# Performance work log

Hardware: AMD Instinct MI355X
Metric: run time of the kernel (lower is better)

## Reference

```python
import jax, jax.numpy as jnp
import numpy as np
from jax import lax

KS = [3, 5, 7, 9]
DS = [1, 2, 3, 4]
BN_EPS = 1e-5


def setup_inputs() -> dict:
    key = jax.random.key(0)
    ks = jax.random.split(key, 16)
    B, Cin, H, W = 16, 64, 256, 256
    Ce = 64  # out_channels // 2
    inp = {"x": jax.random.normal(ks[0], (B, Cin, H, W), jnp.float32)}
    for i, (k, _) in enumerate(zip(KS, DS)):
        fan_in = Cin * k * k
        inp[f"w{i}"] = jax.random.normal(ks[1 + i], (Ce, Cin, k, k), jnp.float32) / np.sqrt(fan_in)
        inp[f"b{i}"] = jnp.zeros((Ce,), jnp.float32)
    inp["bn_scale"] = jnp.ones((4, Ce), jnp.float32)
    inp["bn_bias"] = jnp.zeros((4, Ce), jnp.float32)
    inp["bn_mean"] = jax.random.normal(ks[5], (4, Ce), jnp.float32) * 0.1
    inp["bn_var"] = jax.random.uniform(ks[6], (4, Ce), jnp.float32, 0.5, 1.5)
    inp["gate_w"] = jax.random.normal(ks[7], (4, Cin), jnp.float32) / np.sqrt(Cin)
    inp["gate_b"] = jnp.zeros((4,), jnp.float32)
    return inp


def _expert(x, w, b, scale, bias, mean, var, k, d):
    pad = d * (k - 1) // 2
    y = lax.conv_general_dilated(
        x, w, window_strides=(2, 2), padding=[(pad, pad), (pad, pad)],
        rhs_dilation=(d, d), dimension_numbers=("NCHW", "OIHW", "NCHW"))
    y = y + b[None, :, None, None]
    inv = scale * lax.rsqrt(var + BN_EPS)
    y = y * inv[None, :, None, None] + (bias - mean * inv)[None, :, None, None]
    return jax.nn.gelu(y, approximate=False)


def reference(x, w0, b0, w1, b1, w2, b2, w3, b3,
              bn_scale, bn_bias, bn_mean, bn_var, gate_w, gate_b):
    B = x.shape[0]
    # Gate: global average pool -> linear -> softmax -> top-2 renormalized
    pooled = x.mean(axis=(2, 3))                    # (B, Cin)
    gates = jax.nn.softmax(pooled @ gate_w.T + gate_b, axis=1)  # (B, 4)
    top2_w, top2_idx = lax.top_k(gates, 2)
    top2_w = top2_w / (top2_w.sum(axis=1, keepdims=True) + 1e-8)
    # Dense compute of all 4 experts (faithful to original module)
    ws, bs = [w0, w1, w2, w3], [b0, b1, b2, b3]
    outs = [
        _expert(x, ws[i], bs[i], bn_scale[i], bn_bias[i], bn_mean[i], bn_var[i], KS[i], DS[i])
        for i in range(4)
    ]
    E = jnp.stack(outs, axis=1)                     # (B, 4, Ce, H/2, W/2)
    sel = jnp.take_along_axis(E, top2_idx[:, :, None, None, None], axis=1)  # (B,2,Ce,h,w)
    weighted = sel * top2_w[:, :, None, None, None]
    # concat top-2 along channel dim == reshape (B,2,Ce,h,w) -> (B,2*Ce,h,w)
    Bc, two, Ce, h, w = weighted.shape
    return weighted.reshape(Bc, two * Ce, h, w)
```

## Files before the change

### kernel.cpp

```cpp
#include <hip/hip_runtime.h>
#include <hip/hip_bf16.h>
#include <math.h>

#define CIN 64
#define CE  64
#define HH  256
#define WW  256
#define OHW 128
#define PW  288
#define PH  288

typedef __attribute__((ext_vector_type(8))) short bf16x8;
typedef __attribute__((ext_vector_type(4))) float f32x4;

static __device__ __forceinline__ unsigned short f2bf(float f) {
    __hip_bfloat16 h = __float2bfloat16(f);
    return *reinterpret_cast<unsigned short*>(&h);
}

#define GLOAD16(gsrc, ldst)                                                        \
    __builtin_amdgcn_global_load_lds(                                              \
        (const __attribute__((address_space(1))) void*)(gsrc),                     \
        (__attribute__((address_space(3))) void*)(ldst), 16, 0, 0)

template <bool PRE>
__global__ __launch_bounds__(256)
void poolcvt_kernel(const float* __restrict__ x, unsigned short* __restrict__ xbf,
                    float* __restrict__ partial) {
    int blk = blockIdx.x;
    int rc = blockIdx.y;
    int tid = threadIdx.x, lane = tid & 63, wv = tid >> 6;
    int c0 = lane * 4;
    const float* xb = x + (size_t)blk * 8 * (HH * WW);
    unsigned short* pl = xbf + (size_t)blk * (PW * PH) * 8;
    float s[8];
#pragma unroll
    for (int j = 0; j < 8; ++j) s[j] = 0.f;
#pragma unroll 1
    for (int rr = wv; rr < 32; rr += 4) {
        int h = rc * 32 + rr;
        float4 v[8];
#pragma unroll
        for (int j = 0; j < 8; ++j)
            v[j] = *reinterpret_cast<const float4*>(xb + (size_t)j * (HH * WW) + h * WW + c0);
#pragma unroll
        for (int j = 0; j < 8; ++j) s[j] += (v[j].x + v[j].y) + (v[j].z + v[j].w);
        if (PRE) {
            size_t o16 = ((size_t)(16 + h) * PW + 16 + c0);
            unsigned short u[4][8];
#pragma unroll
            for (int j = 0; j < 8; ++j) {
                u[0][j] = f2bf(v[j].x);
                u[1][j] = f2bf(v[j].y);
                u[2][j] = f2bf(v[j].z);
                u[3][j] = f2bf(v[j].w);
            }
#pragma unroll
            for (int cc = 0; cc < 4; ++cc)
                *reinterpret_cast<bf16x8*>(pl + (o16 + cc) * 8) =
                    *reinterpret_cast<const bf16x8*>(u[cc]);
        }
    }
    if (PRE) {
        bf16x8 z = (bf16x8)(short)0;
#pragma unroll 1
        for (int i = tid; i < 32 * 32; i += 256) {
            int rr = i >> 5, cc = i & 31;
            int pr = 16 + rc * 32 + rr;
            int pc = (cc < 16) ? cc : (256 + cc);
            *reinterpret_cast<bf16x8*>(pl + ((size_t)pr * PW + pc) * 8) = z;
        }
        if (rc == 0) {
#pragma unroll 1
            for (int i = tid; i < 16 * PW; i += 256)
                *reinterpret_cast<bf16x8*>(pl + (size_t)i * 8) = z;
        }
        if (rc == 7) {
#pragma unroll 1
            for (int i = tid; i < 16 * PW; i += 256)
                *reinterpret_cast<bf16x8*>(pl + ((size_t)(272 * PW) + i) * 8) = z;
        }
    }
#pragma unroll
    for (int j = 0; j < 8; ++j) {
#pragma unroll
        for (int m = 32; m >= 1; m >>= 1) s[j] += __shfl_xor(s[j], m, 64);
    }
    __shared__ float red[4][8];
    if (lane == 0) {
#pragma unroll
        for (int j = 0; j < 8; ++j) red[wv][j] = s[j];
    }
    __syncthreads();
    if (tid < 8) {
        int j = tid;
        float t = (red[0][j] + red[1][j]) + (red[2][j] + red[3][j]);
        partial[(blk * 8 + rc) * 8 + j] = t;
    }
}

__global__ __launch_bounds__(64)
void gate_kernel(const float* __restrict__ partial, const float* __restrict__ gw,
                 const float* __restrict__ gb, int* __restrict__ sel_idx,
                 float* __restrict__ sel_w) {
    int b = blockIdx.x;
    int c = threadIdx.x;
    float p = 0.f;
#pragma unroll
    for (int rc = 0; rc < 8; ++rc)
        p += partial[(((b * 8 + (c >> 3)) * 8) + rc) * 8 + (c & 7)];
    p *= (1.0f / (HH * WW));
    float l[4];
#pragma unroll
    for (int e = 0; e < 4; ++e) l[e] = p * gw[e * CIN + c];
#pragma unroll
    for (int m = 32; m >= 1; m >>= 1) {
#pragma unroll
        for (int e = 0; e < 4; ++e) l[e] += __shfl_xor(l[e], m, 64);
    }
    if (c == 0) {
        float g[4], s = 0.f;
#pragma unroll
        for (int e = 0; e < 4; ++e) l[e] += gb[e];
        float mx = fmaxf(fmaxf(l[0], l[1]), fmaxf(l[2], l[3]));
#pragma unroll
        for (int e = 0; e < 4; ++e) { g[e] = expf(l[e] - mx); s += g[e]; }
#pragma unroll
        for (int e = 0; e < 4; ++e) g[e] /= s;
        int i1 = 0;
        for (int e = 1; e < 4; ++e) if (g[e] > g[i1]) i1 = e;
        int i2 = -1;
        for (int e = 0; e < 4; ++e) {
            if (e == i1) continue;
            if (i2 < 0 || g[e] > g[i2]) i2 = e;
        }
        float den = g[i1] + g[i2] + 1e-8f;
        sel_idx[b * 2 + 0] = i1;
        sel_idx[b * 2 + 1] = i2;
        sel_w[b * 2 + 0] = g[i1] / den;
        sel_w[b * 2 + 1] = g[i2] / den;
    }
}

__global__ void order_kernel(const int* __restrict__ sel_idx, int* __restrict__ ord) {
    if (threadIdx.x == 0) {
        int pos = 0;
        const int pri[4] = {3, 2, 1, 0};
        for (int pi = 0; pi < 4; ++pi)
            for (int bs = 0; bs < 32; ++bs)
                if (sel_idx[bs] == pri[pi]) ord[pos++] = bs;
    }
}

__global__ __launch_bounds__(256)
void wprep_all_kernel(const float* __restrict__ w0, const float* __restrict__ w1,
                      const float* __restrict__ w2, const float* __restrict__ w3,
                      unsigned short* __restrict__ wq) {
    int cb = blockIdx.x;
    int y = blockIdx.y;
    const float* w;
    int g0, k, GE;
    size_t base;
    if (y < 3)       { w = w0; g0 = y;      k = 3; GE = 3;  base = 0; }
    else if (y < 10) { w = w1; g0 = y - 3;  k = 5; GE = 7;  base = 49152; }
    else if (y < 23) { w = w2; g0 = y - 10; k = 7; GE = 13; base = 163840; }
    else             { w = w3; g0 = y - 23; k = 9; GE = 21; base = 376832; }
    int k2 = k * k;
    int t = threadIdx.x, tl = t >> 6, co = t & 63;
    int tap = g0 * 4 + tl;
    unsigned short vals[8];
#pragma unroll
    for (int j = 0; j < 8; ++j) {
        float v = 0.f;
        if (tap < k2) v = w[(size_t)(co * CIN + cb * 8 + j) * k2 + tap];
        vals[j] = f2bf(v);
    }
    *reinterpret_cast<bf16x8*>(&wq[base + (size_t)(cb * GE + g0) * 2048 + t * 8]) =
        *reinterpret_cast<const bf16x8*>(vals);
}

template <int K, int D, int GE, bool EVEN, bool PRE>
__device__ __forceinline__ void conv_body(const float* __restrict__ xb,
                                          const unsigned short* __restrict__ xpb,
                                          const unsigned short* __restrict__ wq,
                                          unsigned short* __restrict__ xt,
                                          f32x4 acc[4][4],
                                          int ih0, int iw0, int lane, int wv, int tid) {
    constexpr int K2 = K * K;
    constexpr int TS = 31 + (K - 1) * D;
    constexpr int S = (TS + 1) / 2;
    constexpr int HPW = S * 8;
    constexpr int PITCH = 2 * HPW;
    constexpr int NRC = (TS + 1) / 2;
    constexpr int NEL = EVEN ? NRC * NRC : TS * 2 * S;
    constexpr int DH = EVEN ? D / 2 : 0;
    int p = lane & 15, hi = lane >> 4;

#pragma unroll 1
    for (int cb = 0; cb < 8; ++cb) {
        __syncthreads();
        if constexpr (PRE) {
            const unsigned short* xp = xpb + (size_t)cb * (PW * PH) * 8;
#pragma unroll 1
            for (int idx = tid; idx < NEL; idx += 256) {
                int ih, iw;
                if constexpr (EVEN) {
                    int r = idx / NRC, c = idx - r * NRC;
                    ih = ih0 + 16 + 2 * r;
                    iw = iw0 + 16 + 2 * c;
                } else {
                    int r = idx / (2 * S), rem = idx - r * (2 * S);
                    int half = rem >= S ? 1 : 0;
                    int sl = rem - half * S;
                    int c = 2 * sl + half;
                    c = min(c, TS - 1);
                    ih = ih0 + 16 + r;
                    iw = iw0 + 16 + c;
                }
                GLOAD16(xp + ((size_t)ih * PW + iw) * 8, &xt[idx * 8]);
            }
        } else {
            const float* xc8 = xb + (size_t)cb * 8 * (HH * WW);
#pragma unroll 1
            for (int idx = tid; idx < NEL; idx += 256) {
                int ih, iw;
                if constexpr (EVEN) {
                    int r = idx / NRC, c = idx - r * NRC;
                    ih = ih0 + 2 * r; iw = iw0 + 2 * c;
                } else {
                    int r = idx / (2 * S), rem = idx - r * (2 * S);
                    int half = rem >= S ? 1 : 0;
                    int sl = rem - half * S;
                    int c = min(2 * sl + half, TS - 1);
                    ih = ih0 + r; iw = iw0 + c;
                }
                int ihc = min(max(ih, 0), HH - 1), iwc = min(max(iw, 0), WW - 1);
                bool ok = ((unsigned)ih < (unsigned)HH) && ((unsigned)iw < (unsigned)WW);
                unsigned short u[8];
                const float* src = xc8 + ihc * WW + iwc;
#pragma unroll
                for (int j = 0; j < 8; ++j) u[j] = f2bf(ok ? src[(size_t)j * (HH * WW)] : 0.f);
                *reinterpret_cast<bf16x8*>(&xt[idx * 8]) = *reinterpret_cast<const bf16x8*>(u);
            }
        }
        __syncthreads();
        const unsigned short* wcb = wq + (size_t)cb * GE * 2048;
#pragma unroll 2
        for (int g = 0; g < GE; ++g) {
            int tap = g * 4 + hi;
            int tapc = tap < K2 ? tap : K2 - 1;
            int kh = tapc / K, kw = tapc % K;
            const unsigned short* wg = wcb + g * 2048 + hi * 512;
            bf16x8 a0 = *reinterpret_cast<const bf16x8*>(wg + p * 8);
            bf16x8 a1 = *reinterpret_cast<const bf16x8*>(wg + 128 + p * 8);
            bf16x8 a2 = *reinterpret_cast<const bf16x8*>(wg + 256 + p * 8);
            bf16x8 a3 = *reinterpret_cast<const bf16x8*>(wg + 384 + p * 8);
            if constexpr (EVEN) {
                int ec = p + DH * kw;
                int erb = wv * 4 + DH * kh;
#pragma unroll
                for (int j = 0; j < 4; ++j) {
                    const bf16x8 bf = *reinterpret_cast<const bf16x8*>(
                        &xt[((erb + j) * NRC + ec) * 8]);
                    acc[j][0] = __builtin_amdgcn_mfma_f32_16x16x32_bf16(a0, bf, acc[j][0], 0, 0, 0);
                    acc[j][1] = __builtin_amdgcn_mfma_f32_16x16x32_bf16(a1, bf, acc[j][1], 0, 0, 0);
                    acc[j][2] = __builtin_amdgcn_mfma_f32_16x16x32_bf16(a2, bf, acc[j][2], 0, 0, 0);
                    acc[j][3] = __builtin_amdgcn_mfma_f32_16x16x32_bf16(a3, bf, acc[j][3], 0, 0, 0);
                }
            } else {
                int ic = 2 * p + D * kw;
                int bbase = (ic & 1) * HPW + (ic >> 1) * 8;
                int irb = D * kh + wv * 8;
#pragma unroll
                for (int j = 0; j < 4; ++j) {
                    const bf16x8 bf = *reinterpret_cast<const bf16x8*>(
                        &xt[(irb + 2 * j) * PITCH + bbase]);
                    acc[j][0] = __builtin_amdgcn_mfma_f32_16x16x32_bf16(a0, bf, acc[j][0], 0, 0, 0);
                    acc[j][1] = __builtin_amdgcn_mfma_f32_16x16x32_bf16(a1, bf, acc[j][1], 0, 0, 0);
                    acc[j][2] = __builtin_amdgcn_mfma_f32_16x16x32_bf16(a2, bf, acc[j][2], 0, 0, 0);
                    acc[j][3] = __builtin_amdgcn_mfma_f32_16x16x32_bf16(a3, bf, acc[j][3], 0, 0, 0);
                }
            }
        }
    }
}

template <bool PRE>
__global__ __launch_bounds__(256, 4)
void conv_moe_kernel(const float* __restrict__ x, const unsigned short* __restrict__ xbf,
                     const unsigned short* __restrict__ wq,
                     const float* __restrict__ b0_, const float* __restrict__ b1_,
                     const float* __restrict__ b2_, const float* __restrict__ b3_,
                     const float* __restrict__ bns, const float* __restrict__ bnb,
                     const float* __restrict__ bnm, const float* __restrict__ bnv,
                     const int* __restrict__ sel_idx, const float* __restrict__ sel_w,
                     const int* __restrict__ ord, float* __restrict__ out) {
    __shared__ __align__(16) unsigned short xt[19600];

    int bidx = blockIdx.x;
    int bs = ord[bidx >> 6];
    int tile = bidx & 63;
    int b = bs >> 1, slot = bs & 1;
    int e = sel_idx[bs];
    float gwt = sel_w[bs];
    int oh0 = (tile >> 3) * 16, ow0 = (tile & 7) * 16;
    const float* xb = x + (size_t)b * CIN * HH * WW;
    const unsigned short* xpb = xbf + (size_t)b * 8 * (PW * PH) * 8;
    int tid = threadIdx.x, lane = tid & 63, wv = tid >> 6;
    int p = lane & 15, hi = lane >> 4;

    f32x4 acc[4][4];
#pragma unroll
    for (int j = 0; j < 4; ++j)
#pragma unroll
        for (int ct = 0; ct < 4; ++ct) acc[j][ct] = (f32x4){0.f, 0.f, 0.f, 0.f};

    switch (e) {
        case 0:
            conv_body<3, 1, 3, false, PRE>(xb, xpb, wq, xt, acc, oh0 * 2 - 1, ow0 * 2 - 1, lane, wv, tid);
            break;
        case 1:
            conv_body<5, 2, 7, true, PRE>(xb, xpb, wq + 49152, xt, acc, oh0 * 2 - 4, ow0 * 2 - 4, lane, wv, tid);
            break;
        case 2:
            conv_body<7, 3, 13, false, PRE>(xb, xpb, wq + 163840, xt, acc, oh0 * 2 - 9, ow0 * 2 - 9, lane, wv, tid);
            break;
        default:
            conv_body<9, 4, 21, true, PRE>(xb, xpb, wq + 376832, xt, acc, oh0 * 2 - 16, ow0 * 2 - 16, lane, wv, tid);
            break;
    }

    const float* be = (e == 0) ? b0_ : (e == 1) ? b1_ : (e == 2) ? b2_ : b3_;
    float* ob = out + (size_t)(b * 128 + slot * 64) * (OHW * OHW);
#pragma unroll
    for (int ct = 0; ct < 4; ++ct) {
#pragma unroll
        for (int reg = 0; reg < 4; ++reg) {
            int co = ct * 16 + hi * 4 + reg;
            float bias = be[co];
            float sc = bns[e * CE + co], bi = bnb[e * CE + co];
            float mn = bnm[e * CE + co], vr = bnv[e * CE + co];
            float inv = sc * rsqrtf(vr + 1e-5f);
            float beta = bi - mn * inv + bias * inv;
#pragma unroll
            for (int j = 0; j < 4; ++j) {
                float y = acc[j][ct][reg] * inv + beta;
                float gl = 0.5f * y * (1.0f + erff(y * 0.70710678118654752f));
                int oh = oh0 + wv * 4 + j, ow = ow0 + p;
                ob[(size_t)co * (OHW * OHW) + oh * OHW + ow] = gl * gwt;
            }
        }
    }
}

extern "C" void kernel_launch(void* const* d_in, const int* in_sizes, int n_in,
                              void* d_out, int out_size, void* d_ws, size_t ws_size,
                              hipStream_t stream) {
    const float* x   = (const float*)d_in[0];
    const float* w0  = (const float*)d_in[1];
    const float* b0  = (const float*)d_in[2];
    const float* w1  = (const float*)d_in[3];
    const float* b1  = (const float*)d_in[4];
    const float* w2  = (const float*)d_in[5];
    const float* b2  = (const float*)d_in[6];
    const float* w3  = (const float*)d_in[7];
    const float* b3  = (const float*)d_in[8];
    const float* bns = (const float*)d_in[9];
    const float* bnb = (const float*)d_in[10];
    const float* bnm = (const float*)d_in[11];
    const float* bnv = (const float*)d_in[12];
    const float* gw  = (const float*)d_in[13];
    const float* gb  = (const float*)d_in[14];
    float* out = (float*)d_out;

    char* ws = (char*)d_ws;
    float* partial = (float*)ws;
    int* sel_idx   = (int*)(ws + 32768);
    float* sel_w   = (float*)(ws + 32896);
    int* ord       = (int*)(ws + 33024);
    unsigned short* wq = (unsigned short*)(ws + 33280);
    unsigned short* xbf = (unsigned short*)(ws + 2097152);
    const size_t NEED = 2097152ull + (size_t)128 * PW * PH * 16;
    bool pre = ws_size >= NEED;

    if (pre) poolcvt_kernel<true><<<dim3(128, 8), 256, 0, stream>>>(x, xbf, partial);
    else     poolcvt_kernel<false><<<dim3(128, 8), 256, 0, stream>>>(x, xbf, partial);
    gate_kernel<<<dim3(16), 64, 0, stream>>>(partial, gw, gb, sel_idx, sel_w);
    order_kernel<<<dim3(1), 64, 0, stream>>>(sel_idx, ord);
    wprep_all_kernel<<<dim3(8, 44), 256, 0, stream>>>(w0, w1, w2, w3, wq);

    if (pre)
        conv_moe_kernel<true><<<dim3(2048), 256, 0, stream>>>(
            x, xbf, wq, b0, b1, b2, b3, bns, bnb, bnm, bnv, sel_idx, sel_w, ord, out);
    else
        conv_moe_kernel<false><<<dim3(2048), 256, 0, stream>>>(
            x, xbf, wq, b0, b1, b2, b3, bns, bnb, bnm, bnv, sel_idx, sel_w, ord, out);
}
```

Measured before the change: 305.2 us.

## Register-prefetch next channel block's input tile during MFMA compute

Replaces direct global-to-LDS loads with register staging. The next channel block's tile is loaded into registers while MFMAs run on the current LDS tile, and its global offsets are precomputed once outside the loop. This is meant to hide global load latency behind compute. In exchange it raises register pressure (ITER bf16x8 values per thread), so launch bounds drop from 4 to 3 blocks per SM, which lowers occupancy.

```diff
diff --git a/kernel.cpp b/kernel.cpp
--- a/kernel.cpp
+++ b/kernel.cpp
@@ -17,11 +17,6 @@
     __hip_bfloat16 h = __float2bfloat16(f);
     return *reinterpret_cast<unsigned short*>(&h);
 }
-
-#define GLOAD16(gsrc, ldst)                                                        \
-    __builtin_amdgcn_global_load_lds(                                              \
-        (const __attribute__((address_space(1))) void*)(gsrc),                     \
-        (__attribute__((address_space(3))) void*)(ldst), 16, 0, 0)
 
 template <bool PRE>
 __global__ __launch_bounds__(256)
@@ -193,33 +188,96 @@
     constexpr int PITCH = 2 * HPW;
     constexpr int NRC = (TS + 1) / 2;
     constexpr int NEL = EVEN ? NRC * NRC : TS * 2 * S;
+    constexpr int ITER = (NEL + 255) / 256;
     constexpr int DH = EVEN ? D / 2 : 0;
+    constexpr size_t PLANE = (size_t)PW * PH * 8;
     int p = lane & 15, hi = lane >> 4;
 
-#pragma unroll 1
-    for (int cb = 0; cb < 8; ++cb) {
-        __syncthreads();
-        if constexpr (PRE) {
-            const unsigned short* xp = xpb + (size_t)cb * (PW * PH) * 8;
-#pragma unroll 1
-            for (int idx = tid; idx < NEL; idx += 256) {
-                int ih, iw;
+    if constexpr (PRE) {
+        int gofs[ITER];
+#pragma unroll
+        for (int i = 0; i < ITER; ++i) {
+            int idx = tid + i * 256;
+            if (idx > NEL - 1) idx = NEL - 1;
+            int ih, iw;
+            if constexpr (EVEN) {
+                int r = idx / NRC, c = idx - r * NRC;
+                ih = ih0 + 16 + 2 * r;
+                iw = iw0 + 16 + 2 * c;
+            } else {
+                int r = idx / (2 * S), rem = idx - r * (2 * S);
+                int half = rem >= S ? 1 : 0;
+                int sl = rem - half * S;
+                int c = 2 * sl + half;
+                if (c > TS - 1) c = TS - 1;
+                ih = ih0 + 16 + r;
+                iw = iw0 + 16 + c;
+            }
+            gofs[i] = (ih * PW + iw) * 8;
+        }
+        bf16x8 st[ITER];
+#pragma unroll
+        for (int i = 0; i < ITER; ++i)
+            st[i] = *reinterpret_cast<const bf16x8*>(xpb + gofs[i]);
+
+#pragma unroll 1
+        for (int cb = 0; cb < 8; ++cb) {
+            __syncthreads();
+#pragma unroll
+            for (int i = 0; i < ITER; ++i) {
+                int idx = tid + i * 256;
+                if (idx < NEL) *reinterpret_cast<bf16x8*>(&xt[idx * 8]) = st[i];
+            }
+            __syncthreads();
+            if (cb < 7) {
+                const unsigned short* pn = xpb + (size_t)(cb + 1) * PLANE;
+#pragma unroll
+                for (int i = 0; i < ITER; ++i)
+                    st[i] = *reinterpret_cast<const bf16x8*>(pn + gofs[i]);
+            }
+            const unsigned short* wcb = wq + (size_t)cb * GE * 2048;
+#pragma unroll 2
+            for (int g = 0; g < GE; ++g) {
+                int tap = g * 4 + hi;
+                int tapc = tap < K2 ? tap : K2 - 1;
+                int kh = tapc / K, kw = tapc % K;
+                const unsigned short* wg = wcb + g * 2048 + hi * 512;
+                bf16x8 a0 = *reinterpret_cast<const bf16x8*>(wg + p * 8);
+                bf16x8 a1 = *reinterpret_cast<const bf16x8*>(wg + 128 + p * 8);
+                bf16x8 a2 = *reinterpret_cast<const bf16x8*>(wg + 256 + p * 8);
+                bf16x8 a3 = *reinterpret_cast<const bf16x8*>(wg + 384 + p * 8);
                 if constexpr (EVEN) {
-                    int r = idx / NRC, c = idx - r * NRC;
-                    ih = ih0 + 16 + 2 * r;
-                    iw = iw0 + 16 + 2 * c;
+                    int ec = p + DH * kw;
+                    int erb = wv * 4 + DH * kh;
+#pragma unroll
+                    for (int j = 0; j < 4; ++j) {
+                        const bf16x8 bf = *reinterpret_cast<const bf16x8*>(
+                            &xt[((erb + j) * NRC + ec) * 8]);
+                        acc[j][0] = __builtin_amdgcn_mfma_f32_16x16x32_bf16(a0, bf, acc[j][0], 0, 0, 0);
+                        acc[j][1] = __builtin_amdgcn_mfma_f32_16x16x32_bf16(a1, bf, acc[j][1], 0, 0, 0);
+                        acc[j][2] = __builtin_amdgcn_mfma_f32_16x16x32_bf16(a2, bf, acc[j][2], 0, 0, 0);
+                        acc[j][3] = __builtin_amdgcn_mfma_f32_16x16x32_bf16(a3, bf, acc[j][3], 0, 0, 0);
+                    }
                 } else {
-                    int r = idx / (2 * S), rem = idx - r * (2 * S);
-                    int half = rem >= S ? 1 : 0;
-                    int sl = rem - half * S;
-                    int c = 2 * sl + half;
-                    c = min(c, TS - 1);
-                    ih = ih0 + 16 + r;
-                    iw = iw0 + 16 + c;
+                    int ic = 2 * p + D * kw;
+                    int bbase = (ic & 1) * HPW + (ic >> 1) * 8;
+                    int irb = D * kh + wv * 8;
+#pragma unroll
+                    for (int j = 0; j < 4; ++j) {
+                        const bf16x8 bf = *reinterpret_cast<const bf16x8*>(
+                            &xt[(irb + 2 * j) * PITCH + bbase]);
+                        acc[j][0] = __builtin_amdgcn_mfma_f32_16x16x32_bf16(a0, bf, acc[j][0], 0, 0, 0);
+                        acc[j][1] = __builtin_amdgcn_mfma_f32_16x16x32_bf16(a1, bf, acc[j][1], 0, 0, 0);
+                        acc[j][2] = __builtin_amdgcn_mfma_f32_16x16x32_bf16(a2, bf, acc[j][2], 0, 0, 0);
+                        acc[j][3] = __builtin_amdgcn_mfma_f32_16x16x32_bf16(a3, bf, acc[j][3], 0, 0, 0);
+                    }
                 }
-                GLOAD16(xp + ((size_t)ih * PW + iw) * 8, &xt[idx * 8]);
-            }
-        } else {
+            }
+        }
+    } else {
+#pragma unroll 1
+        for (int cb = 0; cb < 8; ++cb) {
+            __syncthreads();
             const float* xc8 = xb + (size_t)cb * 8 * (HH * WW);
 #pragma unroll 1
             for (int idx = tid; idx < NEL; idx += 256) {
@@ -242,51 +300,51 @@
                 for (int j = 0; j < 8; ++j) u[j] = f2bf(ok ? src[(size_t)j * (HH * WW)] : 0.f);
                 *reinterpret_cast<bf16x8*>(&xt[idx * 8]) = *reinterpret_cast<const bf16x8*>(u);
             }
-        }
-        __syncthreads();
-        const unsigned short* wcb = wq + (size_t)cb * GE * 2048;
+            __syncthreads();
+            const unsigned short* wcb = wq + (size_t)cb * GE * 2048;
 #pragma unroll 2
-        for (int g = 0; g < GE; ++g) {
-            int tap = g * 4 + hi;
-            int tapc = tap < K2 ? tap : K2 - 1;
-            int kh = tapc / K, kw = tapc % K;
-            const unsigned short* wg = wcb + g * 2048 + hi * 512;
-            bf16x8 a0 = *reinterpret_cast<const bf16x8*>(wg + p * 8);
-            bf16x8 a1 = *reinterpret_cast<const bf16x8*>(wg + 128 + p * 8);
-            bf16x8 a2 = *reinterpret_cast<const bf16x8*>(wg + 256 + p * 8);
-            bf16x8 a3 = *reinterpret_cast<const bf16x8*>(wg + 384 + p * 8);
-            if constexpr (EVEN) {
-                int ec = p + DH * kw;
-                int erb = wv * 4 + DH * kh;
-#pragma unroll
-                for (int j = 0; j < 4; ++j) {
-                    const bf16x8 bf = *reinterpret_cast<const bf16x8*>(
-                        &xt[((erb + j) * NRC + ec) * 8]);
-                    acc[j][0] = __builtin_amdgcn_mfma_f32_16x16x32_bf16(a0, bf, acc[j][0], 0, 0, 0);
-                    acc[j][1] = __builtin_amdgcn_mfma_f32_16x16x32_bf16(a1, bf, acc[j][1], 0, 0, 0);
-                    acc[j][2] = __builtin_amdgcn_mfma_f32_16x16x32_bf16(a2, bf, acc[j][2], 0, 0, 0);
-                    acc[j][3] = __builtin_amdgcn_mfma_f32_16x16x32_bf16(a3, bf, acc[j][3], 0, 0, 0);
+            for (int g = 0; g < GE; ++g) {
+                int tap = g * 4 + hi;
+                int tapc = tap < K2 ? tap : K2 - 1;
+                int kh = tapc / K, kw = tapc % K;
+                const unsigned short* wg = wcb + g * 2048 + hi * 512;
+                bf16x8 a0 = *reinterpret_cast<const bf16x8*>(wg + p * 8);
+                bf16x8 a1 = *reinterpret_cast<const bf16x8*>(wg + 128 + p * 8);
+                bf16x8 a2 = *reinterpret_cast<const bf16x8*>(wg + 256 + p * 8);
+                bf16x8 a3 = *reinterpret_cast<const bf16x8*>(wg + 384 + p * 8);
+                if constexpr (EVEN) {
+                    int ec = p + DH * kw;
+                    int erb = wv * 4 + DH * kh;
+#pragma unroll
+                    for (int j = 0; j < 4; ++j) {
+                        const bf16x8 bf = *reinterpret_cast<const bf16x8*>(
+                            &xt[((erb + j) * NRC + ec) * 8]);
+                        acc[j][0] = __builtin_amdgcn_mfma_f32_16x16x32_bf16(a0, bf, acc[j][0], 0, 0, 0);
+                        acc[j][1] = __builtin_amdgcn_mfma_f32_16x16x32_bf16(a1, bf, acc[j][1], 0, 0, 0);
+                        acc[j][2] = __builtin_amdgcn_mfma_f32_16x16x32_bf16(a2, bf, acc[j][2], 0, 0, 0);
+                        acc[j][3] = __builtin_amdgcn_mfma_f32_16x16x32_bf16(a3, bf, acc[j][3], 0, 0, 0);
+                    }
+                } else {
+                    int ic = 2 * p + D * kw;
+                    int bbase = (ic & 1) * HPW + (ic >> 1) * 8;
+                    int irb = D * kh + wv * 8;
+#pragma unroll
+                    for (int j = 0; j < 4; ++j) {
+                        const bf16x8 bf = *reinterpret_cast<const bf16x8*>(
+                            &xt[(irb + 2 * j) * PITCH + bbase]);
+                        acc[j][0] = __builtin_amdgcn_mfma_f32_16x16x32_bf16(a0, bf, acc[j][0], 0, 0, 0);
+                        acc[j][1] = __builtin_amdgcn_mfma_f32_16x16x32_bf16(a1, bf, acc[j][1], 0, 0, 0);
+                        acc[j][2] = __builtin_amdgcn_mfma_f32_16x16x32_bf16(a2, bf, acc[j][2], 0, 0, 0);
+                        acc[j][3] = __builtin_amdgcn_mfma_f32_16x16x32_bf16(a3, bf, acc[j][3], 0, 0, 0);
+                    }
                 }
-            } else {
-                int ic = 2 * p + D * kw;
-                int bbase = (ic & 1) * HPW + (ic >> 1) * 8;
-                int irb = D * kh + wv * 8;
-#pragma unroll
-                for (int j = 0; j < 4; ++j) {
-                    const bf16x8 bf = *reinterpret_cast<const bf16x8*>(
-                        &xt[(irb + 2 * j) * PITCH + bbase]);
-                    acc[j][0] = __builtin_amdgcn_mfma_f32_16x16x32_bf16(a0, bf, acc[j][0], 0, 0, 0);
-                    acc[j][1] = __builtin_amdgcn_mfma_f32_16x16x32_bf16(a1, bf, acc[j][1], 0, 0, 0);
-                    acc[j][2] = __builtin_amdgcn_mfma_f32_16x16x32_bf16(a2, bf, acc[j][2], 0, 0, 0);
-                    acc[j][3] = __builtin_amdgcn_mfma_f32_16x16x32_bf16(a3, bf, acc[j][3], 0, 0, 0);
-                }
             }
         }
     }
 }
 
 template <bool PRE>
-__global__ __launch_bounds__(256, 4)
+__global__ __launch_bounds__(256, 3)
 void conv_moe_kernel(const float* __restrict__ x, const unsigned short* __restrict__ xbf,
                      const unsigned short* __restrict__ wq,
                      const float* __restrict__ b0_, const float* __restrict__ b1_,
```

After: 307.1 us. Within noise of the previous version (+0.6%).

## Stage conv weights through double-buffered LDS with async loads in PRE path

Applied to the files above, without the earlier changes.

In the prepadded-bf16 path, each weight group is now copied into a double-buffered LDS region with global_load_lds, one group ahead of the MFMA loop. MFMA A-operands are read from LDS instead of directly from global memory. A manual vmcnt wait plus barrier per group replaces the two syncthreads per channel block, and tap indices are stepped incrementally instead of recomputed with divisions. The input tile load is now only waited on at the first group barrier, so it can overlap with that barrier point. The cost is a full barrier per weight group, 8 KB more LDS per block, and launch bounds dropped from 4 to 3 blocks per CU, which lowers occupancy.

```diff
diff --git a/kernel.cpp b/kernel.cpp
--- a/kernel.cpp
+++ b/kernel.cpp
@@ -9,6 +9,7 @@
 #define OHW 128
 #define PW  288
 #define PH  288
+#define WOFF 19600
 
 typedef __attribute__((ext_vector_type(8))) short bf16x8;
 typedef __attribute__((ext_vector_type(4))) float f32x4;
@@ -183,7 +184,7 @@
 __device__ __forceinline__ void conv_body(const float* __restrict__ xb,
                                           const unsigned short* __restrict__ xpb,
                                           const unsigned short* __restrict__ wq,
-                                          unsigned short* __restrict__ xt,
+                                          unsigned short* __restrict__ lds,
                                           f32x4 acc[4][4],
                                           int ih0, int iw0, int lane, int wv, int tid) {
     constexpr int K2 = K * K;
@@ -194,12 +195,19 @@
     constexpr int NRC = (TS + 1) / 2;
     constexpr int NEL = EVEN ? NRC * NRC : TS * 2 * S;
     constexpr int DH = EVEN ? D / 2 : 0;
+    constexpr int NPH = 8 * GE;
     int p = lane & 15, hi = lane >> 4;
 
-#pragma unroll 1
-    for (int cb = 0; cb < 8; ++cb) {
-        __syncthreads();
-        if constexpr (PRE) {
+    if constexpr (PRE) {
+        GLOAD16(wq + tid * 8, &lds[WOFF + tid * 8]);
+        const unsigned short* wrun = wq + 2048;
+        int ph = 1;
+        int par = 0;
+
+#pragma unroll 1
+        for (int cb = 0; cb < 8; ++cb) {
+            asm volatile("s_waitcnt vmcnt(0)" ::: "memory");
+            __builtin_amdgcn_s_barrier();
             const unsigned short* xp = xpb + (size_t)cb * (PW * PH) * 8;
 #pragma unroll 1
             for (int idx = tid; idx < NEL; idx += 256) {
@@ -213,13 +221,64 @@
                     int half = rem >= S ? 1 : 0;
                     int sl = rem - half * S;
                     int c = 2 * sl + half;
-                    c = min(c, TS - 1);
+                    if (c > TS - 1) c = TS - 1;
                     ih = ih0 + 16 + r;
                     iw = iw0 + 16 + c;
                 }
-                GLOAD16(xp + ((size_t)ih * PW + iw) * 8, &xt[idx * 8]);
-            }
-        } else {
+                GLOAD16(xp + ((size_t)ih * PW + iw) * 8, &lds[idx * 8]);
+            }
+            int kh = hi / K, kw = hi % K;
+#pragma unroll 2
+            for (int g = 0; g < GE; ++g) {
+                asm volatile("s_waitcnt vmcnt(0)" ::: "memory");
+                __builtin_amdgcn_s_barrier();
+                if (ph < NPH) {
+                    GLOAD16(wrun + tid * 8, &lds[WOFF + (par ^ 1) * 2048 + tid * 8]);
+                    wrun += 2048;
+                    ++ph;
+                }
+                const unsigned short* wl = &lds[WOFF + par * 2048 + hi * 512 + p * 8];
+                bf16x8 a0 = *reinterpret_cast<const bf16x8*>(wl);
+                bf16x8 a1 = *reinterpret_cast<const bf16x8*>(wl + 128);
+                bf16x8 a2 = *reinterpret_cast<const bf16x8*>(wl + 256);
+                bf16x8 a3 = *reinterpret_cast<const bf16x8*>(wl + 384);
+                int khc = min(kh, K - 1);
+                if constexpr (EVEN) {
+                    int ec = p + DH * kw;
+                    int erb = wv * 4 + DH * khc;
+#pragma unroll
+                    for (int j = 0; j < 4; ++j) {
+                        const bf16x8 bf = *reinterpret_cast<const bf16x8*>(
+                            &lds[((erb + j) * NRC + ec) * 8]);
+                        acc[j][0] = __builtin_amdgcn_mfma_f32_16x16x32_bf16(a0, bf, acc[j][0], 0, 0, 0);
+                        acc[j][1] = __builtin_amdgcn_mfma_f32_16x16x32_bf16(a1, bf, acc[j][1], 0, 0, 0);
+                        acc[j][2] = __builtin_amdgcn_mfma_f32_16x16x32_bf16(a2, bf, acc[j][2], 0, 0, 0);
+                        acc[j][3] = __builtin_amdgcn_mfma_f32_16x16x32_bf16(a3, bf, acc[j][3], 0, 0, 0);
+                    }
+                } else {
+                    int ic = 2 * p + D * kw;
+                    int bbase = (ic & 1) * HPW + (ic >> 1) * 8;
+                    int irb = D * khc + wv * 8;
+#pragma unroll
+                    for (int j = 0; j < 4; ++j) {
+                        const bf16x8 bf = *reinterpret_cast<const bf16x8*>(
+                            &lds[(irb + 2 * j) * PITCH + bbase]);
+                        acc[j][0] = __builtin_amdgcn_mfma_f32_16x16x32_bf16(a0, bf, acc[j][0], 0, 0, 0);
+                        acc[j][1] = __builtin_amdgcn_mfma_f32_16x16x32_bf16(a1, bf, acc[j][1], 0, 0, 0);
+                        acc[j][2] = __builtin_amdgcn_mfma_f32_16x16x32_bf16(a2, bf, acc[j][2], 0, 0, 0);
+                        acc[j][3] = __builtin_amdgcn_mfma_f32_16x16x32_bf16(a3, bf, acc[j][3], 0, 0, 0);
+                    }
+                }
+                kw += 4;
+                if (kw >= K) { kw -= K; ++kh; }
+                if (K == 3 && kw >= K) { kw -= K; ++kh; }
+                par ^= 1;
+            }
+        }
+    } else {
+#pragma unroll 1
+        for (int cb = 0; cb < 8; ++cb) {
+            __syncthreads();
             const float* xc8 = xb + (size_t)cb * 8 * (HH * WW);
 #pragma unroll 1
             for (int idx = tid; idx < NEL; idx += 256) {
@@ -240,53 +299,53 @@
                 const float* src = xc8 + ihc * WW + iwc;
 #pragma unroll
                 for (int j = 0; j < 8; ++j) u[j] = f2bf(ok ? src[(size_t)j * (HH * WW)] : 0.f);
-                *reinterpret_cast<bf16x8*>(&xt[idx * 8]) = *reinterpret_cast<const bf16x8*>(u);
-            }
-        }
-        __syncthreads();
-        const unsigned short* wcb = wq + (size_t)cb * GE * 2048;
+                *reinterpret_cast<bf16x8*>(&lds[idx * 8]) = *reinterpret_cast<const bf16x8*>(u);
+            }
+            __syncthreads();
+            const unsigned short* wcb = wq + (size_t)cb * GE * 2048;
 #pragma unroll 2
-        for (int g = 0; g < GE; ++g) {
-            int tap = g * 4 + hi;
-            int tapc = tap < K2 ? tap : K2 - 1;
-            int kh = tapc / K, kw = tapc % K;
-            const unsigned short* wg = wcb + g * 2048 + hi * 512;
-            bf16x8 a0 = *reinterpret_cast<const bf16x8*>(wg + p * 8);
-            bf16x8 a1 = *reinterpret_cast<const bf16x8*>(wg + 128 + p * 8);
-            bf16x8 a2 = *reinterpret_cast<const bf16x8*>(wg + 256 + p * 8);
-            bf16x8 a3 = *reinterpret_cast<const bf16x8*>(wg + 384 + p * 8);
-            if constexpr (EVEN) {
-                int ec = p + DH * kw;
-                int erb = wv * 4 + DH * kh;
-#pragma unroll
-                for (int j = 0; j < 4; ++j) {
-                    const bf16x8 bf = *reinterpret_cast<const bf16x8*>(
-                        &xt[((erb + j) * NRC + ec) * 8]);
-                    acc[j][0] = __builtin_amdgcn_mfma_f32_16x16x32_bf16(a0, bf, acc[j][0], 0, 0, 0);
-                    acc[j][1] = __builtin_amdgcn_mfma_f32_16x16x32_bf16(a1, bf, acc[j][1], 0, 0, 0);
-                    acc[j][2] = __builtin_amdgcn_mfma_f32_16x16x32_bf16(a2, bf, acc[j][2], 0, 0, 0);
-                    acc[j][3] = __builtin_amdgcn_mfma_f32_16x16x32_bf16(a3, bf, acc[j][3], 0, 0, 0);
+            for (int g = 0; g < GE; ++g) {
+                int tap = g * 4 + hi;
+                int tapc = tap < K2 ? tap : K2 - 1;
+                int kh = tapc / K, kw = tapc % K;
+                const unsigned short* wg = wcb + g * 2048 + hi * 512;
+                bf16x8 a0 = *reinterpret_cast<const bf16x8*>(wg + p * 8);
+                bf16x8 a1 = *reinterpret_cast<const bf16x8*>(wg + 128 + p * 8);
+                bf16x8 a2 = *reinterpret_cast<const bf16x8*>(wg + 256 + p * 8);
+                bf16x8 a3 = *reinterpret_cast<const bf16x8*>(wg + 384 + p * 8);
+                if constexpr (EVEN) {
+                    int ec = p + (D / 2) * kw;
+                    int erb = wv * 4 + (D / 2) * kh;
+#pragma unroll
+                    for (int j = 0; j < 4; ++j) {
+                        const bf16x8 bf = *reinterpret_cast<const bf16x8*>(
+                            &lds[((erb + j) * NRC + ec) * 8]);
+                        acc[j][0] = __builtin_amdgcn_mfma_f32_16x16x32_bf16(a0, bf, acc[j][0], 0, 0, 0);
+                        acc[j][1] = __builtin_amdgcn_mfma_f32_16x16x32_bf16(a1, bf, acc[j][1], 0, 0, 0);
+                        acc[j][2] = __builtin_amdgcn_mfma_f32_16x16x32_bf16(a2, bf, acc[j][2], 0, 0, 0);
+                        acc[j][3] = __builtin_amdgcn_mfma_f32_16x16x32_bf16(a3, bf, acc[j][3], 0, 0, 0);
+                    }
+                } else {
+                    int ic = 2 * p + D * kw;
+                    int bbase = (ic & 1) * HPW + (ic >> 1) * 8;
+                    int irb = D * kh + wv * 8;
+#pragma unroll
+                    for (int j = 0; j < 4; ++j) {
+                        const bf16x8 bf = *reinterpret_cast<const bf16x8*>(
+                            &lds[(irb + 2 * j) * PITCH + bbase]);
+                        acc[j][0] = __builtin_amdgcn_mfma_f32_16x16x32_bf16(a0, bf, acc[j][0], 0, 0, 0);
+                        acc[j][1] = __builtin_amdgcn_mfma_f32_16x16x32_bf16(a1, bf, acc[j][1], 0, 0, 0);
+                        acc[j][2] = __builtin_amdgcn_mfma_f32_16x16x32_bf16(a2, bf, acc[j][2], 0, 0, 0);
+                        acc[j][3] = __builtin_amdgcn_mfma_f32_16x16x32_bf16(a3, bf, acc[j][3], 0, 0, 0);
+                    }
                 }
-            } else {
-                int ic = 2 * p + D * kw;
-                int bbase = (ic & 1) * HPW + (ic >> 1) * 8;
-                int irb = D * kh + wv * 8;
-#pragma unroll
-                for (int j = 0; j < 4; ++j) {
-                    const bf16x8 bf = *reinterpret_cast<const bf16x8*>(
-                        &xt[(irb + 2 * j) * PITCH + bbase]);
-                    acc[j][0] = __builtin_amdgcn_mfma_f32_16x16x32_bf16(a0, bf, acc[j][0], 0, 0, 0);
-                    acc[j][1] = __builtin_amdgcn_mfma_f32_16x16x32_bf16(a1, bf, acc[j][1], 0, 0, 0);
-                    acc[j][2] = __builtin_amdgcn_mfma_f32_16x16x32_bf16(a2, bf, acc[j][2], 0, 0, 0);
-                    acc[j][3] = __builtin_amdgcn_mfma_f32_16x16x32_bf16(a3, bf, acc[j][3], 0, 0, 0);
-                }
             }
         }
     }
 }
 
 template <bool PRE>
-__global__ __launch_bounds__(256, 4)
+__global__ __launch_bounds__(256, 3)
 void conv_moe_kernel(const float* __restrict__ x, const unsigned short* __restrict__ xbf,
                      const unsigned short* __restrict__ wq,
                      const float* __restrict__ b0_, const float* __restrict__ b1_,
@@ -295,7 +354,7 @@
                      const float* __restrict__ bnm, const float* __restrict__ bnv,
                      const int* __restrict__ sel_idx, const float* __restrict__ sel_w,
                      const int* __restrict__ ord, float* __restrict__ out) {
-    __shared__ __align__(16) unsigned short xt[19600];
+    __shared__ __align__(16) unsigned short lds[WOFF + 4096];
 
     int bidx = blockIdx.x;
     int bs = ord[bidx >> 6];
@@ -317,16 +376,16 @@
 
     switch (e) {
         case 0:
-            conv_body<3, 1, 3, false, PRE>(xb, xpb, wq, xt, acc, oh0 * 2 - 1, ow0 * 2 - 1, lane, wv, tid);
+            conv_body<3, 1, 3, false, PRE>(xb, xpb, wq, lds, acc, oh0 * 2 - 1, ow0 * 2 - 1, lane, wv, tid);
             break;
         case 1:
-            conv_body<5, 2, 7, true, PRE>(xb, xpb, wq + 49152, xt, acc, oh0 * 2 - 4, ow0 * 2 - 4, lane, wv, tid);
+            conv_body<5, 2, 7, true, PRE>(xb, xpb, wq + 49152, lds, acc, oh0 * 2 - 4, ow0 * 2 - 4, lane, wv, tid);
             break;
         case 2:
-            conv_body<7, 3, 13, false, PRE>(xb, xpb, wq + 163840, xt, acc, oh0 * 2 - 9, ow0 * 2 - 9, lane, wv, tid);
+            conv_body<7, 3, 13, false, PRE>(xb, xpb, wq + 163840, lds, acc, oh0 * 2 - 9, ow0 * 2 - 9, lane, wv, tid);
             break;
         default:
-            conv_body<9, 4, 21, true, PRE>(xb, xpb, wq + 376832, xt, acc, oh0 * 2 - 16, ow0 * 2 - 16, lane, wv, tid);
+            conv_body<9, 4, 21, true, PRE>(xb, xpb, wq + 376832, lds, acc, oh0 * 2 - 16, ow0 * 2 - 16, lane, wv, tid);
             break;
     }
 
```

Measured after the change: 284.7 us. 1.07x faster.
